# Performance work log

Measured on AMD Instinct MI355X. Metric: run time of the kernel, lower is better.

The kernel has to match this reference:

```python
import jax, jax.numpy as jnp
import numpy as np

B, S, D = 4, 4096, 1024
H, DH, F = 16, 64, 64
DFF = 4096
EPS_LN = 1e-5
EPS_ATTN = 1e-6


def setup_inputs() -> dict:
    key = jax.random.key(0)
    ks = jax.random.split(key, 12)
    s = 1.0 / np.sqrt(D)
    inp = {
        'x': jax.random.normal(ks[0], (B, S, D), dtype=jnp.float32),
        'ln1_g': jnp.ones((D,), jnp.float32),
        'ln1_b': jnp.zeros((D,), jnp.float32),
        'wq': jax.random.normal(ks[1], (D, H * DH), jnp.float32) * s,
        'wk': jax.random.normal(ks[2], (D, H * DH), jnp.float32) * s,
        'wv': jax.random.normal(ks[3], (D, H * DH), jnp.float32) * s,
        'proj': jax.random.normal(ks[4], (DH, F), jnp.float32) / np.sqrt(F),
        'wo': jax.random.normal(ks[5], (H * DH, D), jnp.float32) * s,
        'bo': jnp.zeros((D,), jnp.float32),
        'ln2_g': jnp.ones((D,), jnp.float32),
        'ln2_b': jnp.zeros((D,), jnp.float32),
        'w1': jax.random.normal(ks[6], (D, DFF), jnp.float32) * s,
        'b1': jnp.zeros((DFF,), jnp.float32),
        'w2': jax.random.normal(ks[7], (DFF, D), jnp.float32) / np.sqrt(DFF),
        'b2': jnp.zeros((D,), jnp.float32),
    }
    return inp


def _layernorm(x, g, b):
    mu = jnp.mean(x, axis=-1, keepdims=True)
    var = jnp.mean(jnp.square(x - mu), axis=-1, keepdims=True)
    return (x - mu) * jax.lax.rsqrt(var + EPS_LN) * g + b


def _heads(t):  # [B,S,H*DH] -> [B,H,S,DH]
    return t.reshape(B, S, H, DH).transpose(0, 2, 1, 3)


def _feature_map(t, proj):  # [B,H,S,DH] -> [B,H,S,F]
    return jax.nn.relu(jnp.einsum('bhnd,df->bhnf', t, proj)) + EPS_ATTN


def reference(x, ln1_g, ln1_b, wq, wk, wv, proj, wo, bo, ln2_g, ln2_b, w1, b1, w2, b2):
    h = _layernorm(x, ln1_g, ln1_b)
    q = _feature_map(_heads(h @ wq), proj)
    k = _feature_map(_heads(h @ wk), proj)
    v = _heads(h @ wv)
    kv = jnp.einsum('bhnf,bhnd->bhfd', k, v)          # [B,H,F,DH]
    k_sum = k.sum(axis=-2)                            # [B,H,F]
    num = jnp.einsum('bhnf,bhfd->bhnd', q, kv)        # [B,H,S,DH]
    den = jnp.einsum('bhnf,bhf->bhn', q, k_sum) + EPS_ATTN
    attn = num / den[..., None]
    attn = attn.transpose(0, 2, 1, 3).reshape(B, S, H * DH)
    x = x + attn @ wo + bo
    h2 = _layernorm(x, ln2_g, ln2_b)
    ffn = jax.nn.gelu(h2 @ w1 + b1, approximate=False) @ w2 + b2
    return x + ffn
```

## Files before the change

### kernel.cpp

```cpp
#include <hip/hip_runtime.h>
#include <hip/hip_bf16.h>
#include <math.h>

using bf16 = __hip_bfloat16;
typedef __attribute__((ext_vector_type(8))) short short8;
typedef __attribute__((ext_vector_type(4))) float f32x4;

constexpr int Bc = 4, Sc = 4096, Dc = 1024, Hc = 16, DHc = 64, Fc = 64, DFFc = 4096;
constexpr float EPS_LN_C = 1e-5f, EPS_ATTN_C = 1e-6f;
constexpr int KVSPLIT = 16;

static __device__ __forceinline__ float b2f(bf16 v) { return __bfloat162float(v); }
static __device__ __forceinline__ bf16 f2b(float f) { return __float2bfloat16(f); }

__device__ float block_reduce_sum(float v) {
  __shared__ float red[4];
  int lane = threadIdx.x & 63, wid = threadIdx.x >> 6;
#pragma unroll
  for (int off = 32; off > 0; off >>= 1) v += __shfl_down(v, off, 64);
  __syncthreads();
  if (lane == 0) red[wid] = v;
  __syncthreads();
  return red[0] + red[1] + red[2] + red[3];
}

__global__ void ln_kernel(const float* __restrict__ x, const float* __restrict__ g,
                          const float* __restrict__ bta, bf16* __restrict__ out) {
  int row = blockIdx.x;
  const float* xr = x + (size_t)row * Dc;
  int t = threadIdx.x;
  float v[4];
#pragma unroll
  for (int i = 0; i < 4; ++i) v[i] = xr[t + 256 * i];
  float s = block_reduce_sum(v[0] + v[1] + v[2] + v[3]);
  float mu = s * (1.f / Dc);
  float vs = 0.f;
#pragma unroll
  for (int i = 0; i < 4; ++i) { float d = v[i] - mu; vs += d * d; }
  vs = block_reduce_sum(vs);
  float rstd = rsqrtf(vs * (1.f / Dc) + EPS_LN_C);
  bf16* orow = out + (size_t)row * Dc;
#pragma unroll
  for (int i = 0; i < 4; ++i) {
    int c = t + 256 * i;
    orow[c] = f2b((v[i] - mu) * rstd * g[c] + bta[c]);
  }
}

__global__ void tcvt_kernel(const float* __restrict__ in, bf16* __restrict__ out,
                            int K, int N) {
  __shared__ float t[32][33];
  int n0 = blockIdx.x * 32, k0 = blockIdx.y * 32;
  int tid = threadIdx.x;
#pragma unroll
  for (int i = 0; i < 4; ++i) {
    int idx = tid + 256 * i;
    int r = idx >> 5, c = idx & 31;
    t[r][c] = in[(size_t)(k0 + r) * N + n0 + c];
  }
  __syncthreads();
#pragma unroll
  for (int i = 0; i < 4; ++i) {
    int idx = tid + 256 * i;
    int r = idx >> 5, c = idx & 31;
    out[(size_t)(n0 + r) * K + k0 + c] = f2b(t[c][r]);
  }
}

template <int EPI>
__global__ __launch_bounds__(256, 2)
void mgemm_kernel(const ushort* __restrict__ A, const ushort* __restrict__ Bt,
                  const float* __restrict__ bias, const float* __restrict__ res,
                  float* __restrict__ outF, bf16* __restrict__ outB,
                  int M, int N, int K, int lda, int ldbt) {
  __shared__ ushort As[2][128 * 32];
  __shared__ ushort Bs[2][128 * 32];
  int tid = threadIdx.x;
  int wave = tid >> 6, lane = tid & 63;
  int wm = (wave >> 1) * 64, wn = (wave & 1) * 64;
  int mrow = lane & 15, quad = lane >> 4;

  int nn = gridDim.x, nm = gridDim.y;
  int bid = blockIdx.y * nn + blockIdx.x;
  int mtile, ntile;
  if ((nm & 7) == 0) {
    int xcd = bid & 7, s = bid >> 3;
    int mpx = nm >> 3;
    int mloc = s / nn;
    ntile = s - mloc * nn;
    mtile = xcd * mpx + mloc;
  } else { mtile = blockIdx.y; ntile = blockIdx.x; }
  int row0 = mtile * 128, col0 = ntile * 128;

  const int srow = tid >> 2;
  const int scol = (((tid & 3) ^ ((tid >> 3) & 3)) << 3);
  const ushort* aP = A + (size_t)(row0 + srow) * lda + scol;
  const ushort* bP = Bt + (size_t)(col0 + srow) * ldbt + scol;
  const int dst = tid * 8;

  f32x4 acc[4][4] = {};

  const int cq = ((quad ^ ((mrow >> 1) & 3)) << 3);

  for (int k0 = 0; k0 < K; k0 += 64) {
    __syncthreads();
#pragma unroll
    for (int st = 0; st < 2; ++st) {
#pragma unroll
      for (int l = 0; l < 2; ++l) {
        __builtin_amdgcn_global_load_lds(
            (const __attribute__((address_space(1))) void*)(aP + (size_t)(l * 64) * lda + k0 + st * 32),
            (__attribute__((address_space(3))) void*)(&As[st][l * 2048 + dst]), 16, 0, 0);
        __builtin_amdgcn_global_load_lds(
            (const __attribute__((address_space(1))) void*)(bP + (size_t)(l * 64) * ldbt + k0 + st * 32),
            (__attribute__((address_space(3))) void*)(&Bs[st][l * 2048 + dst]), 16, 0, 0);
      }
    }
    __syncthreads();

    short8 af[2][4], bfv[2][4];
#pragma unroll
    for (int st = 0; st < 2; ++st) {
#pragma unroll
      for (int i = 0; i < 4; ++i)
        af[st][i] = *(const short8*)(&As[st][(wm + i * 16 + mrow) * 32 + cq]);
#pragma unroll
      for (int j = 0; j < 4; ++j)
        bfv[st][j] = *(const short8*)(&Bs[st][(wn + j * 16 + mrow) * 32 + cq]);
    }
#pragma unroll
    for (int i = 0; i < 4; ++i)
#pragma unroll
      for (int j = 0; j < 4; ++j) {
        acc[i][j] = __builtin_amdgcn_mfma_f32_16x16x32_bf16(af[0][i], bfv[0][j], acc[i][j], 0, 0, 0);
        acc[i][j] = __builtin_amdgcn_mfma_f32_16x16x32_bf16(af[1][i], bfv[1][j], acc[i][j], 0, 0, 0);
      }
  }

#pragma unroll
  for (int i = 0; i < 4; ++i) {
#pragma unroll
    for (int j = 0; j < 4; ++j) {
      int rb = row0 + wm + i * 16 + quad * 4;
      int c = col0 + wn + j * 16 + mrow;
#pragma unroll
      for (int r = 0; r < 4; ++r) {
        int rr = rb + r;
        float v = acc[i][j][r];
        if (EPI == 1 || EPI == 2) v += bias[c];
        if (EPI == 3) { if (bias) v += bias[c]; }
        if (EPI == 2) v = 0.5f * v * (1.f + erff(v * 0.70710678118654752f));
        if (EPI == 1 || EPI == 3) v += res[(size_t)rr * N + c];
        if (EPI == 4) {
          outB[((size_t)(c >> 10) * (size_t)(Bc * Sc) + rr) * 1024 + (c & 1023)] = f2b(v);
        } else if (EPI == 0 || EPI == 2) {
          outB[(size_t)rr * N + c] = f2b(v);
        } else {
          outF[(size_t)rr * N + c] = v;
        }
      }
    }
  }
}

__global__ __launch_bounds__(256, 2)
void fm_mfma(const ushort* __restrict__ qin, const ushort* __restrict__ pjt,
             bf16* __restrict__ qf) {
  __shared__ ushort As[256 * 64];
  __shared__ ushort Bs[64 * 64];
  int t = threadIdx.x;
  int wave = t >> 6, lane = t & 63;
  int mrow = lane & 15, quad = lane >> 4;
  int b = blockIdx.z, h = blockIdx.y, s0 = blockIdx.x * 256;
  const ushort* abase = qin + ((size_t)b * Sc + s0) * (Hc * DHc) + h * DHc;

#pragma unroll
  for (int i = 0; i < 8; ++i) {
    int c = t + 256 * i;
    int row = c >> 3, col = (c & 7) * 8;
    __builtin_amdgcn_global_load_lds(
        (const __attribute__((address_space(1))) void*)(abase + (size_t)row * (Hc * DHc) + col),
        (__attribute__((address_space(3))) void*)(As + c * 8), 16, 0, 0);
  }
#pragma unroll
  for (int i = 0; i < 2; ++i) {
    int c = t + 256 * i;
    __builtin_amdgcn_global_load_lds(
        (const __attribute__((address_space(1))) void*)(pjt + c * 8),
        (__attribute__((address_space(3))) void*)(Bs + c * 8), 16, 0, 0);
  }
  __syncthreads();

  f32x4 acc[4][4] = {};
#pragma unroll
  for (int step = 0; step < 2; ++step) {
    short8 af[4], bfv[4];
#pragma unroll
    for (int i = 0; i < 4; ++i)
      af[i] = *(const short8*)(As + (wave * 64 + i * 16 + mrow) * 64 + quad * 8 + step * 32);
#pragma unroll
    for (int j = 0; j < 4; ++j)
      bfv[j] = *(const short8*)(Bs + (j * 16 + mrow) * 64 + quad * 8 + step * 32);
#pragma unroll
    for (int i = 0; i < 4; ++i)
#pragma unroll
      for (int j = 0; j < 4; ++j)
        acc[i][j] = __builtin_amdgcn_mfma_f32_16x16x32_bf16(af[i], bfv[j], acc[i][j], 0, 0, 0);
  }

  size_t obase = ((size_t)(b * Hc + h)) * Sc + s0;
#pragma unroll
  for (int i = 0; i < 4; ++i) {
#pragma unroll
    for (int j = 0; j < 4; ++j) {
      int f = j * 16 + mrow;
#pragma unroll
      for (int r = 0; r < 4; ++r) {
        int s = wave * 64 + i * 16 + quad * 4 + r;
        float v = fmaxf(acc[i][j][r], 0.f) + EPS_ATTN_C;
        qf[(obase + s) * Fc + f] = f2b(v);
      }
    }
  }
}

__global__ __launch_bounds__(256, 2)
void kvp_mfma(const ushort* __restrict__ kf, const ushort* __restrict__ v,
              float* __restrict__ kvp, float* __restrict__ ksump) {
  constexpr int LT = 72;
  __shared__ ushort kfT[64 * LT];
  __shared__ ushort vT[64 * LT];
  int t = threadIdx.x;
  int wave = t >> 6, lane = t & 63;
  int mrow = lane & 15, quad = lane >> 4;
  int split = blockIdx.x, bh = blockIdx.y;
  int b = bh >> 4, h = bh & 15;
  int sbase = split * (Sc / KVSPLIT);

  short8 ones, zero;
#pragma unroll
  for (int i = 0; i < 8; ++i) { ones[i] = (short)0x3F80; zero[i] = 0; }
  short8 bks = (mrow == 0) ? ones : zero;

  f32x4 acc[4] = {};
  f32x4 accks = {};

  for (int sc = 0; sc < Sc / KVSPLIT; sc += 64) {
    __syncthreads();
    int sl = t >> 2, c8 = (t & 3) * 8;
    const ushort* kp = kf + (((size_t)bh * Sc) + sbase + sc + sl) * Fc + c8;
    const ushort* vp = v + (((size_t)b * Sc) + sbase + sc + sl) * (Hc * DHc) + h * DHc + c8;
#pragma unroll
    for (int half = 0; half < 2; ++half) {
      short8 kv8 = *(const short8*)(kp + half * 32);
      short8 vv8 = *(const short8*)(vp + half * 32);
#pragma unroll
      for (int jj = 0; jj < 8; ++jj) {
        kfT[(c8 + half * 32 + jj) * LT + sl] = (ushort)kv8[jj];
        vT[(c8 + half * 32 + jj) * LT + sl] = (ushort)vv8[jj];
      }
    }
    __syncthreads();
#pragma unroll
    for (int step = 0; step < 2; ++step) {
      short8 af = *(const short8*)(kfT + (wave * 16 + mrow) * LT + quad * 8 + step * 32);
      short8 bfv[4];
#pragma unroll
      for (int j = 0; j < 4; ++j)
        bfv[j] = *(const short8*)(vT + (j * 16 + mrow) * LT + quad * 8 + step * 32);
#pragma unroll
      for (int j = 0; j < 4; ++j)
        acc[j] = __builtin_amdgcn_mfma_f32_16x16x32_bf16(af, bfv[j], acc[j], 0, 0, 0);
      accks = __builtin_amdgcn_mfma_f32_16x16x32_bf16(af, bks, accks, 0, 0, 0);
    }
  }

  size_t pbase = (size_t)bh * KVSPLIT + split;
#pragma unroll
  for (int j = 0; j < 4; ++j) {
    int d = j * 16 + mrow;
#pragma unroll
    for (int r = 0; r < 4; ++r) {
      int f = wave * 16 + quad * 4 + r;
      kvp[(pbase * 64 + f) * 64 + d] = acc[j][r];
    }
  }
  if (mrow == 0) {
#pragma unroll
    for (int r = 0; r < 4; ++r) {
      int f = wave * 16 + quad * 4 + r;
      ksump[pbase * 64 + f] = accks[r];
    }
  }
}

__global__ void kvr_kernel(const float* __restrict__ kvp, const float* __restrict__ ksump,
                           bf16* __restrict__ kvt, bf16* __restrict__ ksum16) {
  int bh = blockIdx.x;
  int t = threadIdx.x;
#pragma unroll
  for (int i = 0; i < 16; ++i) {
    int idx = t + 256 * i;
    int f = idx >> 6, d = idx & 63;
    float s = 0.f;
#pragma unroll
    for (int j = 0; j < KVSPLIT; ++j)
      s += kvp[((size_t)bh * KVSPLIT + j) * 4096 + idx];
    kvt[((size_t)bh * 64 + d) * 64 + f] = f2b(s);
  }
  if (t < 64) {
    float s = 0.f;
#pragma unroll
    for (int j = 0; j < KVSPLIT; ++j)
      s += ksump[((size_t)bh * KVSPLIT + j) * 64 + t];
    ksum16[bh * 64 + t] = f2b(s);
  }
}

__global__ __launch_bounds__(256, 2)
void attn_mfma(const ushort* __restrict__ qf, const ushort* __restrict__ kvt,
               const ushort* __restrict__ ksum16, bf16* __restrict__ attn) {
  __shared__ ushort As[256 * 64];
  __shared__ ushort Bs[64 * 64];
  int t = threadIdx.x;
  int wave = t >> 6, lane = t & 63;
  int mrow = lane & 15, quad = lane >> 4;
  int b = blockIdx.z, h = blockIdx.y, s0 = blockIdx.x * 256;
  int bh = b * Hc + h;
  const ushort* abase = qf + (((size_t)bh * Sc) + s0) * Fc;
  const ushort* bbase = kvt + (size_t)bh * 4096;

#pragma unroll
  for (int i = 0; i < 8; ++i) {
    int c = t + 256 * i;
    __builtin_amdgcn_global_load_lds(
        (const __attribute__((address_space(1))) void*)(abase + c * 8),
        (__attribute__((address_space(3))) void*)(As + c * 8), 16, 0, 0);
  }
#pragma unroll
  for (int i = 0; i < 2; ++i) {
    int c = t + 256 * i;
    __builtin_amdgcn_global_load_lds(
        (const __attribute__((address_space(1))) void*)(bbase + c * 8),
        (__attribute__((address_space(3))) void*)(Bs + c * 8), 16, 0, 0);
  }
  short8 zero;
#pragma unroll
  for (int i = 0; i < 8; ++i) zero[i] = 0;
  short8 ksf[2];
#pragma unroll
  for (int step = 0; step < 2; ++step) {
    short8 kv8 = *(const short8*)(ksum16 + bh * 64 + quad * 8 + step * 32);
    ksf[step] = (mrow == 0) ? kv8 : zero;
  }
  __syncthreads();

  f32x4 acc[4][4] = {};
  f32x4 accd[4] = {};
#pragma unroll
  for (int step = 0; step < 2; ++step) {
    short8 af[4], bfv[4];
#pragma unroll
    for (int i = 0; i < 4; ++i)
      af[i] = *(const short8*)(As + (wave * 64 + i * 16 + mrow) * 64 + quad * 8 + step * 32);
#pragma unroll
    for (int j = 0; j < 4; ++j)
      bfv[j] = *(const short8*)(Bs + (j * 16 + mrow) * 64 + quad * 8 + step * 32);
#pragma unroll
    for (int i = 0; i < 4; ++i) {
#pragma unroll
      for (int j = 0; j < 4; ++j)
        acc[i][j] = __builtin_amdgcn_mfma_f32_16x16x32_bf16(af[i], bfv[j], acc[i][j], 0, 0, 0);
      accd[i] = __builtin_amdgcn_mfma_f32_16x16x32_bf16(af[i], ksf[step], accd[i], 0, 0, 0);
    }
  }

#pragma unroll
  for (int i = 0; i < 4; ++i) {
    float inv[4];
#pragma unroll
    for (int r = 0; r < 4; ++r) {
      float den = __shfl(accd[i][r], lane & 48);
      inv[r] = 1.0f / (den + EPS_ATTN_C);
    }
#pragma unroll
    for (int j = 0; j < 4; ++j) {
      int d = j * 16 + mrow;
#pragma unroll
      for (int r = 0; r < 4; ++r) {
        int s = s0 + wave * 64 + i * 16 + quad * 4 + r;
        attn[((size_t)(b * Sc + s)) * (Hc * DHc) + h * DHc + d] = f2b(acc[i][j][r] * inv[r]);
      }
    }
  }
}

extern "C" void kernel_launch(void* const* d_in, const int* in_sizes, int n_in,
                              void* d_out, int out_size, void* d_ws, size_t ws_size,
                              hipStream_t stream) {
  const float* x     = (const float*)d_in[0];
  const float* ln1_g = (const float*)d_in[1];
  const float* ln1_b = (const float*)d_in[2];
  const float* wq    = (const float*)d_in[3];
  const float* wk    = (const float*)d_in[4];
  const float* wv    = (const float*)d_in[5];
  const float* proj  = (const float*)d_in[6];
  const float* wo    = (const float*)d_in[7];
  const float* bo    = (const float*)d_in[8];
  const float* ln2_g = (const float*)d_in[9];
  const float* ln2_b = (const float*)d_in[10];
  const float* w1    = (const float*)d_in[11];
  const float* b1    = (const float*)d_in[12];
  const float* w2    = (const float*)d_in[13];
  const float* b2    = (const float*)d_in[14];
  float* out = (float*)d_out;
  (void)ws_size; (void)in_sizes; (void)n_in; (void)out_size;

  const size_t TOK = (size_t)Bc * Sc;
  const size_t REG = TOK * Dc * sizeof(bf16);
  char* ws = (char*)d_ws;
  bf16* R0 = (bf16*)(ws + 0 * REG);
  bf16* R1 = (bf16*)(ws + 1 * REG);
  bf16* R2 = (bf16*)(ws + 2 * REG);
  bf16* R3 = (bf16*)(ws + 3 * REG);
  bf16* mid = R1;
  float* kvpart = (float*)R2;
  float* kspart = (float*)((char*)R2 + (size_t)64 * KVSPLIT * 4096 * 4);
  char* p = ws + 4 * REG;
  bf16* kvt   = (bf16*)p;                 p += (size_t)64 * 64 * 64 * 2;
  bf16* ksb16 = (bf16*)p;                 p += (size_t)64 * 64 * 2;
  bf16* pjt   = (bf16*)p;                 p += (size_t)64 * 64 * 2;
  bf16* wqt = (bf16*)p;                   p += (size_t)Dc * Dc * 2;
  bf16* wkt = (bf16*)p;                   p += (size_t)Dc * Dc * 2;
  bf16* wvt = (bf16*)p;                   p += (size_t)Dc * Dc * 2;
  bf16* wot = (bf16*)p;                   p += (size_t)Dc * Dc * 2;
  bf16* w1t = (bf16*)p;                   p += (size_t)Dc * DFFc * 2;
  bf16* w2t = (bf16*)p;                   p += (size_t)Dc * DFFc * 2;

  dim3 blk(256);
  tcvt_kernel<<<dim3(Dc / 32, Dc / 32), blk, 0, stream>>>(wq, wqt, Dc, Dc);
  tcvt_kernel<<<dim3(Dc / 32, Dc / 32), blk, 0, stream>>>(wk, wkt, Dc, Dc);
  tcvt_kernel<<<dim3(Dc / 32, Dc / 32), blk, 0, stream>>>(wv, wvt, Dc, Dc);
  tcvt_kernel<<<dim3(Dc / 32, Dc / 32), blk, 0, stream>>>(wo, wot, Dc, Dc);
  tcvt_kernel<<<dim3(DFFc / 32, Dc / 32), blk, 0, stream>>>(w1, w1t, Dc, DFFc);
  tcvt_kernel<<<dim3(Dc / 32, DFFc / 32), blk, 0, stream>>>(w2, w2t, DFFc, Dc);
  tcvt_kernel<<<dim3(2, 2), blk, 0, stream>>>(proj, pjt, 64, 64);

  ln_kernel<<<dim3(TOK), blk, 0, stream>>>(x, ln1_g, ln1_b, R0);

  dim3 gQKV(3072 / 128, TOK / 128);
  mgemm_kernel<4><<<gQKV, blk, 0, stream>>>((const ushort*)R0, (const ushort*)wqt, nullptr, nullptr,
                                            nullptr, R1, TOK, 3072, Dc, Dc, Dc);

  dim3 gF(Sc / 256, Hc, Bc);
  fm_mfma<<<gF, blk, 0, stream>>>((const ushort*)R1, (const ushort*)pjt, R0);
  fm_mfma<<<gF, blk, 0, stream>>>((const ushort*)R2, (const ushort*)pjt, R1);

  kvp_mfma<<<dim3(KVSPLIT, Bc * Hc), blk, 0, stream>>>((const ushort*)R1, (const ushort*)R3,
                                                       kvpart, kspart);
  kvr_kernel<<<dim3(Bc * Hc), blk, 0, stream>>>(kvpart, kspart, kvt, ksb16);

  attn_mfma<<<gF, blk, 0, stream>>>((const ushort*)R0, (const ushort*)kvt,
                                    (const ushort*)ksb16, R2);

  dim3 gD(Dc / 128, TOK / 128);
  mgemm_kernel<1><<<gD, blk, 0, stream>>>((const ushort*)R2, (const ushort*)wot, bo, x,
                                          out, nullptr, TOK, Dc, Dc, Dc, Dc);

  ln_kernel<<<dim3(TOK), blk, 0, stream>>>(out, ln2_g, ln2_b, R0);

  dim3 gW1(2048 / 128, TOK / 128);
  mgemm_kernel<2><<<gW1, blk, 0, stream>>>((const ushort*)R0, (const ushort*)w1t, b1, nullptr,
                                           nullptr, mid, TOK, 2048, Dc, Dc, Dc);
  mgemm_kernel<3><<<gD, blk, 0, stream>>>((const ushort*)mid, (const ushort*)w2t, b2, out,
                                          out, nullptr, TOK, Dc, 2048, 2048, DFFc);
  mgemm_kernel<2><<<gW1, blk, 0, stream>>>((const ushort*)R0, (const ushort*)(w1t + (size_t)2048 * Dc), b1 + 2048,
                                           nullptr, nullptr, mid, TOK, 2048, Dc, Dc, Dc);
  mgemm_kernel<3><<<gD, blk, 0, stream>>>((const ushort*)mid, (const ushort*)(w2t + 2048), nullptr, out,
                                          out, nullptr, TOK, Dc, 2048, 2048, DFFc);
}
```

Measured before the change: 839.1 us.

## Fold feature projection into Q/K weights, vectorize layernorm, split FFN by token halves

Precomputes Wq·proj and Wk·proj on device so the QKV GEMM epilogue applies relu+eps and writes the feature-mapped layout directly, removing both fm_mfma launches and their activation round trips. The layernorm kernel now uses float4 loads and packed bf16 stores. The FFN is split by token halves instead of by hidden-dimension halves, so b2 is added once and the output read-modify-write passes drop from two to one. Folding the projection into the bf16 weights changes where rounding occurs, and the new weight precompute is a scalar FP32 kernel.

```diff
diff --git a/kernel.cpp b/kernel.cpp
--- a/kernel.cpp
+++ b/kernel.cpp
@@ -4,6 +4,7 @@
 
 using bf16 = __hip_bfloat16;
 typedef __attribute__((ext_vector_type(8))) short short8;
+typedef __attribute__((ext_vector_type(4))) short short4v;
 typedef __attribute__((ext_vector_type(4))) float f32x4;
 
 constexpr int Bc = 4, Sc = 4096, Dc = 1024, Hc = 16, DHc = 64, Fc = 64, DFFc = 4096;
@@ -27,11 +28,10 @@
 __global__ void ln_kernel(const float* __restrict__ x, const float* __restrict__ g,
                           const float* __restrict__ bta, bf16* __restrict__ out) {
   int row = blockIdx.x;
-  const float* xr = x + (size_t)row * Dc;
   int t = threadIdx.x;
-  float v[4];
-#pragma unroll
-  for (int i = 0; i < 4; ++i) v[i] = xr[t + 256 * i];
+  const float4* xr = (const float4*)(x + (size_t)row * Dc);
+  float4 v4 = xr[t];
+  float v[4] = {v4.x, v4.y, v4.z, v4.w};
   float s = block_reduce_sum(v[0] + v[1] + v[2] + v[3]);
   float mu = s * (1.f / Dc);
   float vs = 0.f;
@@ -39,12 +39,17 @@
   for (int i = 0; i < 4; ++i) { float d = v[i] - mu; vs += d * d; }
   vs = block_reduce_sum(vs);
   float rstd = rsqrtf(vs * (1.f / Dc) + EPS_LN_C);
-  bf16* orow = out + (size_t)row * Dc;
+  float4 g4 = ((const float4*)g)[t];
+  float4 b4 = ((const float4*)bta)[t];
+  float gg[4] = {g4.x, g4.y, g4.z, g4.w};
+  float bb[4] = {b4.x, b4.y, b4.z, b4.w};
+  short4v o;
 #pragma unroll
   for (int i = 0; i < 4; ++i) {
-    int c = t + 256 * i;
-    orow[c] = f2b((v[i] - mu) * rstd * g[c] + bta[c]);
-  }
+    bf16 h = f2b((v[i] - mu) * rstd * gg[i] + bb[i]);
+    o[i] = *(short*)&h;
+  }
+  *(short4v*)(out + (size_t)row * Dc + t * 4) = o;
 }
 
 __global__ void tcvt_kernel(const float* __restrict__ in, bf16* __restrict__ out,
@@ -65,6 +70,37 @@
     int r = idx >> 5, c = idx & 31;
     out[(size_t)(n0 + r) * K + k0 + c] = f2b(t[c][r]);
   }
+}
+
+__global__ void tcvt_proj_kernel(const float* __restrict__ wq, const float* __restrict__ wk,
+                                 const float* __restrict__ proj,
+                                 bf16* __restrict__ wqpt, bf16* __restrict__ wkpt) {
+  __shared__ float wsl[64][65];
+  __shared__ float ps[64][64];
+  int t = threadIdx.x;
+  int k0 = blockIdx.x * 64, h = blockIdx.y;
+  const float* w = blockIdx.z ? wk : wq;
+  bf16* outp = blockIdx.z ? wkpt : wqpt;
+#pragma unroll
+  for (int i = 0; i < 16; ++i) {
+    int idx = t + 256 * i;
+    int r = idx >> 6, c = idx & 63;
+    wsl[r][c] = w[(size_t)(k0 + r) * (Hc * DHc) + h * DHc + c];
+    ps[r][c] = proj[idx];
+  }
+  __syncthreads();
+  int k = t & 63, fg = t >> 6;
+  float acc[16];
+#pragma unroll
+  for (int i = 0; i < 16; ++i) acc[i] = 0.f;
+  for (int d = 0; d < 64; ++d) {
+    float wv = wsl[k][d];
+#pragma unroll
+    for (int i = 0; i < 16; ++i) acc[i] += wv * ps[d][fg * 16 + i];
+  }
+#pragma unroll
+  for (int i = 0; i < 16; ++i)
+    outp[(size_t)(h * 64 + fg * 16 + i) * Dc + k0 + k] = f2b(acc[i]);
 }
 
 template <int EPI>
@@ -99,7 +135,6 @@
   const int dst = tid * 8;
 
   f32x4 acc[4][4] = {};
-
   const int cq = ((quad ^ ((mrow >> 1) & 3)) << 3);
 
   for (int k0 = 0; k0 < K; k0 += 64) {
@@ -152,73 +187,21 @@
         if (EPI == 2) v = 0.5f * v * (1.f + erff(v * 0.70710678118654752f));
         if (EPI == 1 || EPI == 3) v += res[(size_t)rr * N + c];
         if (EPI == 4) {
-          outB[((size_t)(c >> 10) * (size_t)(Bc * Sc) + rr) * 1024 + (c & 1023)] = f2b(v);
+          int buf = c >> 10;
+          size_t base = (size_t)buf * ((size_t)Bc * Sc * 1024);
+          if (buf < 2) {
+            float vv = fmaxf(v, 0.f) + EPS_ATTN_C;
+            size_t bb = (size_t)(rr >> 12), ss = (size_t)(rr & 4095);
+            int h = (c >> 6) & 15, f = c & 63;
+            outB[base + ((bb * 16 + h) * 4096 + ss) * 64 + f] = f2b(vv);
+          } else {
+            outB[base + (size_t)rr * 1024 + (c & 1023)] = f2b(v);
+          }
         } else if (EPI == 0 || EPI == 2) {
           outB[(size_t)rr * N + c] = f2b(v);
         } else {
           outF[(size_t)rr * N + c] = v;
         }
-      }
-    }
-  }
-}
-
-__global__ __launch_bounds__(256, 2)
-void fm_mfma(const ushort* __restrict__ qin, const ushort* __restrict__ pjt,
-             bf16* __restrict__ qf) {
-  __shared__ ushort As[256 * 64];
-  __shared__ ushort Bs[64 * 64];
-  int t = threadIdx.x;
-  int wave = t >> 6, lane = t & 63;
-  int mrow = lane & 15, quad = lane >> 4;
-  int b = blockIdx.z, h = blockIdx.y, s0 = blockIdx.x * 256;
-  const ushort* abase = qin + ((size_t)b * Sc + s0) * (Hc * DHc) + h * DHc;
-
-#pragma unroll
-  for (int i = 0; i < 8; ++i) {
-    int c = t + 256 * i;
-    int row = c >> 3, col = (c & 7) * 8;
-    __builtin_amdgcn_global_load_lds(
-        (const __attribute__((address_space(1))) void*)(abase + (size_t)row * (Hc * DHc) + col),
-        (__attribute__((address_space(3))) void*)(As + c * 8), 16, 0, 0);
-  }
-#pragma unroll
-  for (int i = 0; i < 2; ++i) {
-    int c = t + 256 * i;
-    __builtin_amdgcn_global_load_lds(
-        (const __attribute__((address_space(1))) void*)(pjt + c * 8),
-        (__attribute__((address_space(3))) void*)(Bs + c * 8), 16, 0, 0);
-  }
-  __syncthreads();
-
-  f32x4 acc[4][4] = {};
-#pragma unroll
-  for (int step = 0; step < 2; ++step) {
-    short8 af[4], bfv[4];
-#pragma unroll
-    for (int i = 0; i < 4; ++i)
-      af[i] = *(const short8*)(As + (wave * 64 + i * 16 + mrow) * 64 + quad * 8 + step * 32);
-#pragma unroll
-    for (int j = 0; j < 4; ++j)
-      bfv[j] = *(const short8*)(Bs + (j * 16 + mrow) * 64 + quad * 8 + step * 32);
-#pragma unroll
-    for (int i = 0; i < 4; ++i)
-#pragma unroll
-      for (int j = 0; j < 4; ++j)
-        acc[i][j] = __builtin_amdgcn_mfma_f32_16x16x32_bf16(af[i], bfv[j], acc[i][j], 0, 0, 0);
-  }
-
-  size_t obase = ((size_t)(b * Hc + h)) * Sc + s0;
-#pragma unroll
-  for (int i = 0; i < 4; ++i) {
-#pragma unroll
-    for (int j = 0; j < 4; ++j) {
-      int f = j * 16 + mrow;
-#pragma unroll
-      for (int r = 0; r < 4; ++r) {
-        int s = wave * 64 + i * 16 + quad * 4 + r;
-        float v = fmaxf(acc[i][j][r], 0.f) + EPS_ATTN_C;
-        qf[(obase + s) * Fc + f] = f2b(v);
       }
     }
   }
@@ -423,13 +406,11 @@
   bf16* R1 = (bf16*)(ws + 1 * REG);
   bf16* R2 = (bf16*)(ws + 2 * REG);
   bf16* R3 = (bf16*)(ws + 3 * REG);
-  bf16* mid = R1;
-  float* kvpart = (float*)R2;
-  float* kspart = (float*)((char*)R2 + (size_t)64 * KVSPLIT * 4096 * 4);
+  float* kvpart = (float*)R0;
+  float* kspart = (float*)((char*)R0 + (size_t)64 * KVSPLIT * 4096 * 4);
   char* p = ws + 4 * REG;
   bf16* kvt   = (bf16*)p;                 p += (size_t)64 * 64 * 64 * 2;
   bf16* ksb16 = (bf16*)p;                 p += (size_t)64 * 64 * 2;
-  bf16* pjt   = (bf16*)p;                 p += (size_t)64 * 64 * 2;
   bf16* wqt = (bf16*)p;                   p += (size_t)Dc * Dc * 2;
   bf16* wkt = (bf16*)p;                   p += (size_t)Dc * Dc * 2;
   bf16* wvt = (bf16*)p;                   p += (size_t)Dc * Dc * 2;
@@ -438,13 +419,11 @@
   bf16* w2t = (bf16*)p;                   p += (size_t)Dc * DFFc * 2;
 
   dim3 blk(256);
-  tcvt_kernel<<<dim3(Dc / 32, Dc / 32), blk, 0, stream>>>(wq, wqt, Dc, Dc);
-  tcvt_kernel<<<dim3(Dc / 32, Dc / 32), blk, 0, stream>>>(wk, wkt, Dc, Dc);
+  tcvt_proj_kernel<<<dim3(Dc / 64, Hc, 2), blk, 0, stream>>>(wq, wk, proj, wqt, wkt);
   tcvt_kernel<<<dim3(Dc / 32, Dc / 32), blk, 0, stream>>>(wv, wvt, Dc, Dc);
   tcvt_kernel<<<dim3(Dc / 32, Dc / 32), blk, 0, stream>>>(wo, wot, Dc, Dc);
   tcvt_kernel<<<dim3(DFFc / 32, Dc / 32), blk, 0, stream>>>(w1, w1t, Dc, DFFc);
   tcvt_kernel<<<dim3(Dc / 32, DFFc / 32), blk, 0, stream>>>(w2, w2t, DFFc, Dc);
-  tcvt_kernel<<<dim3(2, 2), blk, 0, stream>>>(proj, pjt, 64, 64);
 
   ln_kernel<<<dim3(TOK), blk, 0, stream>>>(x, ln1_g, ln1_b, R0);
 
@@ -452,15 +431,12 @@
   mgemm_kernel<4><<<gQKV, blk, 0, stream>>>((const ushort*)R0, (const ushort*)wqt, nullptr, nullptr,
                                             nullptr, R1, TOK, 3072, Dc, Dc, Dc);
 
-  dim3 gF(Sc / 256, Hc, Bc);
-  fm_mfma<<<gF, blk, 0, stream>>>((const ushort*)R1, (const ushort*)pjt, R0);
-  fm_mfma<<<gF, blk, 0, stream>>>((const ushort*)R2, (const ushort*)pjt, R1);
-
-  kvp_mfma<<<dim3(KVSPLIT, Bc * Hc), blk, 0, stream>>>((const ushort*)R1, (const ushort*)R3,
+  kvp_mfma<<<dim3(KVSPLIT, Bc * Hc), blk, 0, stream>>>((const ushort*)R2, (const ushort*)R3,
                                                        kvpart, kspart);
   kvr_kernel<<<dim3(Bc * Hc), blk, 0, stream>>>(kvpart, kspart, kvt, ksb16);
 
-  attn_mfma<<<gF, blk, 0, stream>>>((const ushort*)R0, (const ushort*)kvt,
+  dim3 gF(Sc / 256, Hc, Bc);
+  attn_mfma<<<gF, blk, 0, stream>>>((const ushort*)R1, (const ushort*)kvt,
                                     (const ushort*)ksb16, R2);
 
   dim3 gD(Dc / 128, TOK / 128);
@@ -469,13 +445,14 @@
 
   ln_kernel<<<dim3(TOK), blk, 0, stream>>>(out, ln2_g, ln2_b, R0);
 
-  dim3 gW1(2048 / 128, TOK / 128);
-  mgemm_kernel<2><<<gW1, blk, 0, stream>>>((const ushort*)R0, (const ushort*)w1t, b1, nullptr,
-                                           nullptr, mid, TOK, 2048, Dc, Dc, Dc);
-  mgemm_kernel<3><<<gD, blk, 0, stream>>>((const ushort*)mid, (const ushort*)w2t, b2, out,
-                                          out, nullptr, TOK, Dc, 2048, 2048, DFFc);
-  mgemm_kernel<2><<<gW1, blk, 0, stream>>>((const ushort*)R0, (const ushort*)(w1t + (size_t)2048 * Dc), b1 + 2048,
-                                           nullptr, nullptr, mid, TOK, 2048, Dc, Dc, Dc);
-  mgemm_kernel<3><<<gD, blk, 0, stream>>>((const ushort*)mid, (const ushort*)(w2t + 2048), nullptr, out,
-                                          out, nullptr, TOK, Dc, 2048, 2048, DFFc);
-}
+  bf16* mid = R1;
+  for (int half = 0; half < 2; ++half) {
+    const ushort* a1 = (const ushort*)R0 + (size_t)half * 8192 * Dc;
+    float* outh = out + (size_t)half * 8192 * Dc;
+    mgemm_kernel<2><<<dim3(DFFc / 128, 8192 / 128), blk, 0, stream>>>(
+        a1, (const ushort*)w1t, b1, nullptr, nullptr, mid, 8192, DFFc, Dc, Dc, Dc);
+    mgemm_kernel<3><<<dim3(Dc / 128, 8192 / 128), blk, 0, stream>>>(
+        (const ushort*)mid, (const ushort*)w2t, b2, outh, outh, nullptr,
+        8192, Dc, DFFc, DFFc, DFFc);
+  }
+}
```

Result: no change. 838.8 us (-0.0%).
